# Kernel tuning notes

Measured on AMD Instinct MI355X. Metric: run time of the kernel, lower is better.

## Reference

```python
import jax, jax.numpy as jnp
import numpy as np

N = 100000      # num graph nodes
E = 1600000     # num edges (avg degree 16)
IN = 128        # in_channels
H = 128         # hidden_channels
B = 4096        # query batch
CTX = 20        # context set length (indices[:, 3:])


def setup_inputs() -> dict:
    key = jax.random.key(0)
    ks = jax.random.split(key, 16)
    inp = {
        "indices": jax.random.randint(ks[0], (B, 3 + CTX), 0, N, dtype=jnp.int64),
        "src": jax.random.randint(ks[1], (E,), 0, N, dtype=jnp.int32),
        "dst": jax.random.randint(ks[2], (E,), 0, N, dtype=jnp.int32),
        "w": jax.random.uniform(ks[3], (E,), dtype=jnp.float32),
        # learned params
        "ndata": jax.random.normal(ks[4], (N, IN), dtype=jnp.float32),
        "W1": jax.random.normal(ks[5], (H, IN), dtype=jnp.float32) * (1.0 / np.sqrt(IN)),
        "b1": jnp.zeros((H,), jnp.float32),
        "W2": jax.random.normal(ks[6], (H, H), dtype=jnp.float32) * (1.0 / np.sqrt(H)),
        "b2": jnp.zeros((H,), jnp.float32),
        "eps": jnp.zeros((2,), jnp.float32),  # learn_eps, one per GINConv
        "Wc1": jax.random.normal(ks[7], (H, 3 * H), dtype=jnp.float32) * (1.0 / np.sqrt(3 * H)),
        "bc1": jnp.zeros((H,), jnp.float32),
        "Wc2": jax.random.normal(ks[8], (H // 2, H), dtype=jnp.float32) * (1.0 / np.sqrt(H)),
        "bc2": jnp.zeros((H // 2,), jnp.float32),
        "Wc3": jax.random.normal(ks[9], (1, H // 2), dtype=jnp.float32) * (1.0 / np.sqrt(H // 2)),
        "bc3": jnp.zeros((1,), jnp.float32),
    }
    return inp


def _gin_conv(x, src, dst, w, deg, eps, W, b):
    # DGL GINConv(mean, learn_eps): h = lin((1+eps)*x + mean_{in-edges}(w_e * x_src))
    msg = w[:, None] * x[src]                                   # [E, D]
    agg = jax.ops.segment_sum(msg, dst, num_segments=N) / deg   # [N, D]
    return ((1.0 + eps) * x + agg) @ W.T + b


def reference(indices, src, dst, w, ndata, W1, b1, W2, b2, eps,
              Wc1, bc1, Wc2, bc2, Wc3, bc3):
    deg = jax.ops.segment_sum(jnp.ones((E,), ndata.dtype), dst, num_segments=N)
    deg = jnp.maximum(deg, 1.0)[:, None]

    x = ndata
    x = jax.nn.relu(_gin_conv(x, src, dst, w, deg, eps[0], W1, b1))  # dropout inactive (eval)
    x = _gin_conv(x, src, dst, w, deg, eps[1], W2, b2)               # last layer: no relu
    x = x.at[0].set(0.0)                                             # x[0] = zeros

    ing1 = x[indices[:, 0]]   # [B, H]
    ing2 = x[indices[:, 1]]   # [B, H]

    # embed_context: mean over nonzero-index context members
    ctx_idx = indices[:, 3:]                                   # [B, CTX]
    ctx_sum = x[ctx_idx].sum(axis=1)                           # [B, H]
    norm = jnp.maximum((ctx_idx > 0).sum(axis=1), 1).astype(x.dtype)[:, None]
    ctx = ctx_sum / norm

    y = jnp.concatenate([ing1, ing2, ctx], axis=1)             # [B, 3H]
    y = jax.nn.relu(y @ Wc1.T + bc1)
    y = jax.nn.relu(y @ Wc2.T + bc2)
    y = y @ Wc3.T + bc3                                        # [B, 1]
    return y
```

## Files before the change

kernel.cpp:

```cpp
#include <hip/hip_runtime.h>


#define CONV_NPB 32
#define FIN_EPB 8

__global__ void init_kernel(const float* __restrict__ W1, const float* __restrict__ W2,
                            const float* __restrict__ Wc1, const float* __restrict__ Wc2,
                            float* __restrict__ Wt1, float* __restrict__ Wt2,
                            float* __restrict__ Wc1t, float* __restrict__ Wc2t,
                            int* __restrict__ cnt, int n) {
  int i = blockIdx.x * blockDim.x + threadIdx.x;
  if (i < n) cnt[i] = 0;
  if (i < 16384) {
    int f = i >> 7, k = i & 127;
    Wt1[k * 128 + f] = W1[i];
  } else if (i < 32768) {
    int j = i - 16384; int f = j >> 7, k = j & 127;
    Wt2[k * 128 + f] = W2[j];
  } else if (i < 81920) {
    int j = i - 32768; int f = j / 384, k = j % 384;
    Wc1t[k * 128 + f] = Wc1[j];
  } else if (i < 90112) {
    int j = i - 81920; int f = j >> 7, k = j & 127;
    Wc2t[k * 64 + f] = Wc2[j];
  }
}

__global__ void hist_kernel(const int* __restrict__ dst, int* __restrict__ cnt,
                            int* __restrict__ rank, int E) {
  int e = (blockIdx.x * blockDim.x + threadIdx.x) * 4;
  if (e + 3 < E) {
    const int4 d = *(const int4*)&dst[e];
    int4 r;
    r.x = atomicAdd(&cnt[d.x], 1);
    r.y = atomicAdd(&cnt[d.y], 1);
    r.z = atomicAdd(&cnt[d.z], 1);
    r.w = atomicAdd(&cnt[d.w], 1);
    *(int4*)&rank[e] = r;
  } else {
    for (; e < E; ++e) rank[e] = atomicAdd(&cnt[dst[e]], 1);
  }
}

__global__ void scan1_kernel(const int* __restrict__ cnt, int* __restrict__ prow,
                             int* __restrict__ bsum, int n) {
  __shared__ int smem[256];
  const int t = threadIdx.x;
  const int base = blockIdx.x * 2048 + t * 8;
  int v[8];
  int s = 0;
#pragma unroll
  for (int j = 0; j < 8; ++j) {
    int idx = base + j;
    v[j] = (idx < n) ? ((cnt[idx] + 7) & ~7) : 0;
    s += v[j];
  }
  smem[t] = s;
  __syncthreads();
  for (int off = 1; off < 256; off <<= 1) {
    int add = (t >= off) ? smem[t - off] : 0;
    __syncthreads();
    smem[t] += add;
    __syncthreads();
  }
  int run = smem[t] - s;
  if (t == 255) bsum[blockIdx.x] = smem[255];
#pragma unroll
  for (int j = 0; j < 8; ++j) {
    int idx = base + j;
    if (idx < n) prow[idx] = run;
    run += v[j];
  }
}

__global__ void scan2_kernel(int* __restrict__ bsum, int nb) {
  const int t = threadIdx.x;
  if (nb <= 64) {
    const int orig = (t < nb) ? bsum[t] : 0;
    int v = orig;
#pragma unroll
    for (int off = 1; off < 64; off <<= 1) {
      int u = __shfl_up(v, off);
      if (t >= off) v += u;
    }
    if (t == nb - 1) bsum[nb] = v;
    if (t < nb) bsum[t] = v - orig;
  } else if (t == 0) {
    int run = 0;
    for (int i = 0; i < nb; ++i) { int v = bsum[i]; bsum[i] = run; run += v; }
    bsum[nb] = run;
  }
}

__global__ void scatter_kernel(const int* __restrict__ src, const int* __restrict__ dst,
                               const float* __restrict__ w, const int* __restrict__ prow,
                               const int* __restrict__ bsum, const int* __restrict__ rank,
                               const int* __restrict__ cnt,
                               int2* __restrict__ epack, int E, int n) {
  const int i = blockIdx.x * blockDim.x + threadIdx.x;
  int e = i * 4;
  if (e + 3 < E) {
    const int4 d = *(const int4*)&dst[e];
    const int4 s = *(const int4*)&src[e];
    const float4 wv = *(const float4*)&w[e];
    const int4 r = *(const int4*)&rank[e];
    epack[prow[d.x] + bsum[d.x >> 11] + r.x] = make_int2(s.x, __float_as_int(wv.x));
    epack[prow[d.y] + bsum[d.y >> 11] + r.y] = make_int2(s.y, __float_as_int(wv.y));
    epack[prow[d.z] + bsum[d.z >> 11] + r.z] = make_int2(s.z, __float_as_int(wv.z));
    epack[prow[d.w] + bsum[d.w >> 11] + r.w] = make_int2(s.w, __float_as_int(wv.w));
  } else {
    for (; e < E; ++e) {
      const int d = dst[e];
      epack[prow[d] + bsum[d >> 11] + rank[e]] = make_int2(src[e], __float_as_int(w[e]));
    }
  }
  if (i < n) {
    const int c = cnt[i];
    const int start = prow[i] + bsum[i >> 11] + c;
    const int pc = ((c + 7) & ~7) - c;
    for (int j = 0; j < pc; ++j) epack[start + j] = make_int2(0, 0);
  }
}

__launch_bounds__(256, 8)
__global__ void conv_kernel(const float* __restrict__ xin, float* __restrict__ xout,
                            const int* __restrict__ prow, const int* __restrict__ bsum,
                            const int* __restrict__ cnt,
                            const int2* __restrict__ epack,
                            const float* __restrict__ Wt,
                            const float* __restrict__ bias, const float* __restrict__ eps,
                            int epsidx, int dorelu, int zerorow0, int n, int nchunk) {
  __shared__ float xm[CONV_NPB * 128];
  __shared__ int rp_s[CONV_NPB + 1];
  const int t = threadIdx.x;
  const int nb = blockIdx.x * CONV_NPB;
  const float epsv = 1.0f + eps[epsidx];

#pragma unroll
  for (int i = 0; i < 4; ++i)
    *(float4*)&xm[(t + i * 256) * 4] = make_float4(0.f, 0.f, 0.f, 0.f);
  if (t <= CONV_NPB) {
    const int node = nb + t;
    rp_s[t] = (node >= n) ? bsum[nchunk] : (prow[node] + bsum[node >> 11]);
  }
  __syncthreads();

  {
    const int L = t >> 5;
    const int lane = t & 31;
    const int f0 = lane * 4;
    const int e0 = rp_s[0], eT = rp_s[CONV_NPB];
    const int nbat = (eT - e0) >> 3;
    const int chunk = (((nbat + 7) >> 3)) << 3;
    const int jb = e0 + L * chunk;
    const int je = min(jb + chunk, eT);
    if (jb < je) {
      const int4* ep4 = (const int4*)epack;
      int r = 0;
      while (rp_s[r + 1] <= jb) ++r;
      float4 acc = make_float4(0.f, 0.f, 0.f, 0.f);
      int h = jb >> 1;
      int4 q0 = ep4[h + 0];
      int4 q1 = ep4[h + 1];
      int4 q2 = ep4[h + 2];
      int4 q3 = ep4[h + 3];
      for (int j = jb; j < je; j += 8) {
        if (rp_s[r + 1] <= j) {
          float* bp = &xm[r * 128 + lane];
          atomicAdd(bp + 0,  acc.x);
          atomicAdd(bp + 32, acc.y);
          atomicAdd(bp + 64, acc.z);
          atomicAdd(bp + 96, acc.w);
          acc = make_float4(0.f, 0.f, 0.f, 0.f);
          do { ++r; } while (rp_s[r + 1] <= j);
        }
        const float4 a0 = *(const float4*)&xin[(size_t)q0.x * 128 + f0];
        const float4 a1 = *(const float4*)&xin[(size_t)q0.z * 128 + f0];
        const float4 a2 = *(const float4*)&xin[(size_t)q1.x * 128 + f0];
        const float4 a3 = *(const float4*)&xin[(size_t)q1.z * 128 + f0];
        const float4 a4 = *(const float4*)&xin[(size_t)q2.x * 128 + f0];
        const float4 a5 = *(const float4*)&xin[(size_t)q2.z * 128 + f0];
        const float4 a6 = *(const float4*)&xin[(size_t)q3.x * 128 + f0];
        const float4 a7 = *(const float4*)&xin[(size_t)q3.z * 128 + f0];
        const float w0 = __int_as_float(q0.y), w1 = __int_as_float(q0.w);
        const float w2 = __int_as_float(q1.y), w3 = __int_as_float(q1.w);
        const float w4 = __int_as_float(q2.y), w5 = __int_as_float(q2.w);
        const float w6 = __int_as_float(q3.y), w7 = __int_as_float(q3.w);
        const int jn = (j + 8 < je) ? (j + 8) : j;
        const int hn = jn >> 1;
        q0 = ep4[hn + 0];
        q1 = ep4[hn + 1];
        q2 = ep4[hn + 2];
        q3 = ep4[hn + 3];
        acc.x += w0 * a0.x + w1 * a1.x + w2 * a2.x + w3 * a3.x
               + w4 * a4.x + w5 * a5.x + w6 * a6.x + w7 * a7.x;
        acc.y += w0 * a0.y + w1 * a1.y + w2 * a2.y + w3 * a3.y
               + w4 * a4.y + w5 * a5.y + w6 * a6.y + w7 * a7.y;
        acc.z += w0 * a0.z + w1 * a1.z + w2 * a2.z + w3 * a3.z
               + w4 * a4.z + w5 * a5.z + w6 * a6.z + w7 * a7.z;
        acc.w += w0 * a0.w + w1 * a1.w + w2 * a2.w + w3 * a3.w
               + w4 * a4.w + w5 * a5.w + w6 * a6.w + w7 * a7.w;
      }
      float* bp = &xm[r * 128 + lane];
      atomicAdd(bp + 0,  acc.x);
      atomicAdd(bp + 32, acc.y);
      atomicAdd(bp + 64, acc.z);
      atomicAdd(bp + 96, acc.w);
    }
  }
  __syncthreads();

  {
    float4 m[4];
#pragma unroll
    for (int q = 0; q < 4; ++q) {
      const int task = t + q * 256;
      const int r = task >> 5;
      const int fg = task & 31;
      m[q].x = xm[r * 128 + fg];
      m[q].y = xm[r * 128 + 32 + fg];
      m[q].z = xm[r * 128 + 64 + fg];
      m[q].w = xm[r * 128 + 96 + fg];
    }
    __syncthreads();
#pragma unroll
    for (int q = 0; q < 4; ++q) {
      const int task = t + q * 256;
      const int r = task >> 5;
      const int fg = task & 31;
      const int f0 = fg * 4;
      const int node = nb + r;
      float4 v = make_float4(0.f, 0.f, 0.f, 0.f);
      if (node < n) {
        const int d = cnt[node];
        const float rdeg = 1.0f / (float)(d > 1 ? d : 1);
        const float4 xv = *(const float4*)&xin[(size_t)node * 128 + f0];
        v.x = epsv * xv.x + m[q].x * rdeg;
        v.y = epsv * xv.y + m[q].y * rdeg;
        v.z = epsv * xv.z + m[q].z * rdeg;
        v.w = epsv * xv.w + m[q].w * rdeg;
      }
      *(float4*)&xm[r * 128 + f0] = v;
    }
  }
  __syncthreads();

  {
    const int fg = t & 31;
    const int rg = t >> 5;
    const int f0 = fg * 4;
    const int r0 = rg * 4;
    float4 acc[4];
#pragma unroll
    for (int r = 0; r < 4; ++r) acc[r] = make_float4(0.f, 0.f, 0.f, 0.f);
    for (int k = 0; k < 128; k += 4) {
      const float4 w0 = *(const float4*)&Wt[(k + 0) * 128 + f0];
      const float4 w1 = *(const float4*)&Wt[(k + 1) * 128 + f0];
      const float4 w2 = *(const float4*)&Wt[(k + 2) * 128 + f0];
      const float4 w3 = *(const float4*)&Wt[(k + 3) * 128 + f0];
#pragma unroll
      for (int r = 0; r < 4; ++r) {
        const float4 xv = *(const float4*)&xm[(r0 + r) * 128 + k];
        acc[r].x += xv.x * w0.x + xv.y * w1.x + xv.z * w2.x + xv.w * w3.x;
        acc[r].y += xv.x * w0.y + xv.y * w1.y + xv.z * w2.y + xv.w * w3.y;
        acc[r].z += xv.x * w0.z + xv.y * w1.z + xv.z * w2.z + xv.w * w3.z;
        acc[r].w += xv.x * w0.w + xv.y * w1.w + xv.z * w2.w + xv.w * w3.w;
      }
    }
    const float4 bv = *(const float4*)&bias[f0];
#pragma unroll
    for (int r = 0; r < 4; ++r) {
      const int node = nb + r0 + r;
      if (node < n) {
        float4 v;
        v.x = acc[r].x + bv.x;
        v.y = acc[r].y + bv.y;
        v.z = acc[r].z + bv.z;
        v.w = acc[r].w + bv.w;
        if (dorelu) {
          v.x = fmaxf(v.x, 0.f); v.y = fmaxf(v.y, 0.f);
          v.z = fmaxf(v.z, 0.f); v.w = fmaxf(v.w, 0.f);
        }
        if (zerorow0 && node == 0) { v.x = 0.f; v.y = 0.f; v.z = 0.f; v.w = 0.f; }
        *(float4*)&xout[(size_t)node * 128 + f0] = v;
      }
    }
  }
}

__launch_bounds__(256, 4)
__global__ void final_kernel(const float* __restrict__ x2, const int* __restrict__ indices,
                             const float* __restrict__ Wc1t, const float* __restrict__ bc1,
                             const float* __restrict__ Wc2t, const float* __restrict__ bc2,
                             const float* __restrict__ Wc3, const float* __restrict__ bc3,
                             float* __restrict__ out) {
  __shared__ float ysm[FIN_EPB * 384];
  __shared__ float h1s[FIN_EPB * 128];
  __shared__ float h2s[FIN_EPB * 64];
  __shared__ int ind_s[FIN_EPB * 23];
  __shared__ float ccs[FIN_EPB];
  const int t = threadIdx.x;
  const int b0 = blockIdx.x * FIN_EPB;

  if (t < FIN_EPB * 23) ind_s[t] = indices[(size_t)b0 * 23 + t];
  __syncthreads();
  if (t < FIN_EPB) {
    int cc = 0;
#pragma unroll
    for (int j = 0; j < 20; ++j) cc += (ind_s[t * 23 + 3 + j] > 0) ? 1 : 0;
    ccs[t] = 1.0f / (float)(cc > 0 ? cc : 1);
  }
  __syncthreads();

  {
#pragma unroll
    for (int q = 0; q < 2; ++q) {
      const int s = t + q * 256;
      const int e = s >> 6;
      const int half = (s >> 5) & 1;
      const int fg = s & 31;
      const int idx = ind_s[e * 23 + half];
      *(float4*)&ysm[e * 384 + half * 128 + fg * 4] =
          *(const float4*)&x2[(size_t)idx * 128 + fg * 4];
    }
    const int e = t >> 5;
    const int fg = t & 31;
    float4 acc = make_float4(0.f, 0.f, 0.f, 0.f);
#pragma unroll
    for (int j = 0; j < 20; ++j) {
      const int cj = ind_s[e * 23 + 3 + j];
      const float4 a = *(const float4*)&x2[(size_t)cj * 128 + fg * 4];
      acc.x += a.x; acc.y += a.y; acc.z += a.z; acc.w += a.w;
    }
    const float sc = ccs[e];
    acc.x *= sc; acc.y *= sc; acc.z *= sc; acc.w *= sc;
    *(float4*)&ysm[e * 384 + 256 + fg * 4] = acc;
  }
  __syncthreads();

  {
    const int f1 = t & 127;
    const int eh = t >> 7;
    float acc[4];
    const float b = bc1[f1];
#pragma unroll
    for (int i = 0; i < 4; ++i) acc[i] = b;
    for (int k = 0; k < 384; k += 4) {
      const float wv0 = Wc1t[(k + 0) * 128 + f1];
      const float wv1 = Wc1t[(k + 1) * 128 + f1];
      const float wv2 = Wc1t[(k + 2) * 128 + f1];
      const float wv3 = Wc1t[(k + 3) * 128 + f1];
#pragma unroll
      for (int i = 0; i < 4; ++i) {
        const float4 yv = *(const float4*)&ysm[(eh * 4 + i) * 384 + k];
        acc[i] += yv.x * wv0 + yv.y * wv1 + yv.z * wv2 + yv.w * wv3;
      }
    }
#pragma unroll
    for (int i = 0; i < 4; ++i)
      h1s[(eh * 4 + i) * 128 + f1] = fmaxf(acc[i], 0.f);
  }
  __syncthreads();

  {
    const int f2 = t & 63;
    const int eg = t >> 6;
    float acc[2];
    const float b = bc2[f2];
#pragma unroll
    for (int i = 0; i < 2; ++i) acc[i] = b;
    for (int k = 0; k < 128; k += 4) {
      const float wv0 = Wc2t[(k + 0) * 64 + f2];
      const float wv1 = Wc2t[(k + 1) * 64 + f2];
      const float wv2 = Wc2t[(k + 2) * 64 + f2];
      const float wv3 = Wc2t[(k + 3) * 64 + f2];
#pragma unroll
      for (int i = 0; i < 2; ++i) {
        const float4 hv = *(const float4*)&h1s[(eg * 2 + i) * 128 + k];
        acc[i] += hv.x * wv0 + hv.y * wv1 + hv.z * wv2 + hv.w * wv3;
      }
    }
#pragma unroll
    for (int i = 0; i < 2; ++i)
      h2s[(eg * 2 + i) * 64 + f2] = fmaxf(acc[i], 0.f);
  }
  __syncthreads();

  {
    const int e = t >> 5;
    const int l = t & 31;
    float p = h2s[e * 64 + l] * Wc3[l] + h2s[e * 64 + l + 32] * Wc3[l + 32];
#pragma unroll
    for (int o = 16; o > 0; o >>= 1) p += __shfl_down(p, o, 32);
    if (l == 0) out[b0 + e] = p + bc3[0];
  }
}

extern "C" void kernel_launch(void* const* d_in, const int* in_sizes, int n_in,
                              void* d_out, int out_size, void* d_ws, size_t ws_size,
                              hipStream_t stream) {
  const int* indices = (const int*)d_in[0];
  const int* src = (const int*)d_in[1];
  const int* dst = (const int*)d_in[2];
  const float* w = (const float*)d_in[3];
  const float* ndata = (const float*)d_in[4];
  const float* W1 = (const float*)d_in[5];
  const float* b1 = (const float*)d_in[6];
  const float* W2 = (const float*)d_in[7];
  const float* b2 = (const float*)d_in[8];
  const float* eps = (const float*)d_in[9];
  const float* Wc1 = (const float*)d_in[10];
  const float* bc1 = (const float*)d_in[11];
  const float* Wc2 = (const float*)d_in[12];
  const float* bc2 = (const float*)d_in[13];
  const float* Wc3 = (const float*)d_in[14];
  const float* bc3 = (const float*)d_in[15];
  float* out = (float*)d_out;

  const int E = in_sizes[1];
  const int N = in_sizes[4] / 128;
  const int B = in_sizes[0] / 23;

  char* ws = (char*)d_ws;
  size_t off = 0;
  auto alloc = [&](size_t bytes) -> char* {
    char* p = ws + off;
    off = (off + bytes + 255) & ~(size_t)255;
    return p;
  };
  const size_t Epad = (size_t)E + 8 * (size_t)N;
  int* cnt = (int*)alloc((size_t)N * 4);
  int* prow = (int*)alloc((size_t)(N + 1) * 4);
  int* rank = (int*)alloc((size_t)E * 4);
  int* bsum = (int*)alloc(256 * 4);
  int2* epack = (int2*)alloc(Epad * 8);
  float* x1 = (float*)alloc((size_t)N * 128 * 4);
  float* x2 = (float*)alloc((size_t)N * 128 * 4);
  float* Wt1 = (float*)alloc(16384 * 4);
  float* Wt2 = (float*)alloc(16384 * 4);
  float* Wc1t = (float*)alloc(49152 * 4);
  float* Wc2t = (float*)alloc(8192 * 4);

  const int ninit = (N > 90112) ? N : 90112;
  init_kernel<<<(ninit + 255) / 256, 256, 0, stream>>>(W1, W2, Wc1, Wc2, Wt1, Wt2, Wc1t, Wc2t, cnt, N);
  const int Eq = (E + 3) / 4;
  hist_kernel<<<(Eq + 255) / 256, 256, 0, stream>>>(dst, cnt, rank, E);
  const int nchunk = (N + 2047) / 2048;
  scan1_kernel<<<nchunk, 256, 0, stream>>>(cnt, prow, bsum, N);
  scan2_kernel<<<1, 64, 0, stream>>>(bsum, nchunk);
  const int nsc = (Eq > N) ? Eq : N;
  scatter_kernel<<<(nsc + 255) / 256, 256, 0, stream>>>(src, dst, w, prow, bsum, rank, cnt, epack, E, N);

  const int nconv = (N + CONV_NPB - 1) / CONV_NPB;
  conv_kernel<<<nconv, 256, 0, stream>>>(ndata, x1, prow, bsum, cnt, epack, Wt1, b1, eps, 0, 1, 0, N, nchunk);
  conv_kernel<<<nconv, 256, 0, stream>>>(x1, x2, prow, bsum, cnt, epack, Wt2, b2, eps, 1, 0, 1, N, nchunk);

  final_kernel<<<B / FIN_EPB, 256, 0, stream>>>(x2, indices, Wc1t, bc1, Wc2t, bc2, Wc3, bc3, out);
}
```

Measured before the change: 554.1 us.

## Gather neighbor features in fp16 to halve edge-gather bandwidth

Node features are kept as fp16 copies: ndata is cast during init, and each conv layer writes an fp16 output alongside (or instead of) fp32. The edge gather in the aggregation and the final context gather read the half-precision rows and convert them to float for accumulation. This halves the random-access gather traffic, which is the dominant cost. In exchange it adds a cast pass over ndata, an extra fp16 store in layer 1, and rounding error in the aggregated features.

```diff
diff --git a/kernel.cpp b/kernel.cpp
--- a/kernel.cpp
+++ b/kernel.cpp
@@ -1,16 +1,41 @@
 #include <hip/hip_runtime.h>
+#include <hip/hip_fp16.h>
 
 
 #define CONV_NPB 32
 #define FIN_EPB 8
 
+struct __align__(8)  h4 { __half2 a, b; };
+struct __align__(16) h8 { __half2 a, b, c, d; };
+
+__device__ __forceinline__ float4 h4f(h4 u) {
+  return make_float4(__low2float(u.a), __high2float(u.a),
+                     __low2float(u.b), __high2float(u.b));
+}
+__device__ __forceinline__ h4 f4h(float4 v) {
+  h4 u; u.a = __floats2half2_rn(v.x, v.y); u.b = __floats2half2_rn(v.z, v.w);
+  return u;
+}
+
 __global__ void init_kernel(const float* __restrict__ W1, const float* __restrict__ W2,
                             const float* __restrict__ Wc1, const float* __restrict__ Wc2,
+                            const float* __restrict__ ndata, __half* __restrict__ xh0,
                             float* __restrict__ Wt1, float* __restrict__ Wt2,
                             float* __restrict__ Wc1t, float* __restrict__ Wc2t,
                             int* __restrict__ cnt, int n) {
   int i = blockIdx.x * blockDim.x + threadIdx.x;
   if (i < n) cnt[i] = 0;
+  const int cbase = i * 8;
+  if (cbase < n * 128) {
+    const float4 v0 = *(const float4*)&ndata[cbase];
+    const float4 v1 = *(const float4*)&ndata[cbase + 4];
+    h8 u;
+    u.a = __floats2half2_rn(v0.x, v0.y);
+    u.b = __floats2half2_rn(v0.z, v0.w);
+    u.c = __floats2half2_rn(v1.x, v1.y);
+    u.d = __floats2half2_rn(v1.z, v1.w);
+    *(h8*)&xh0[cbase] = u;
+  }
   if (i < 16384) {
     int f = i >> 7, k = i & 127;
     Wt1[k * 128 + f] = W1[i];
@@ -123,13 +148,15 @@
 }
 
 __launch_bounds__(256, 8)
-__global__ void conv_kernel(const float* __restrict__ xin, float* __restrict__ xout,
+__global__ void conv_kernel(const float* __restrict__ xin, const __half* __restrict__ xinh,
+                            float* __restrict__ xout, __half* __restrict__ xouth,
                             const int* __restrict__ prow, const int* __restrict__ bsum,
                             const int* __restrict__ cnt,
                             const int2* __restrict__ epack,
                             const float* __restrict__ Wt,
                             const float* __restrict__ bias, const float* __restrict__ eps,
-                            int epsidx, int dorelu, int zerorow0, int n, int nchunk) {
+                            int epsidx, int dorelu, int zerorow0, int writef32,
+                            int n, int nchunk) {
   __shared__ float xm[CONV_NPB * 128];
   __shared__ int rp_s[CONV_NPB + 1];
   const int t = threadIdx.x;
@@ -174,14 +201,14 @@
           acc = make_float4(0.f, 0.f, 0.f, 0.f);
           do { ++r; } while (rp_s[r + 1] <= j);
         }
-        const float4 a0 = *(const float4*)&xin[(size_t)q0.x * 128 + f0];
-        const float4 a1 = *(const float4*)&xin[(size_t)q0.z * 128 + f0];
-        const float4 a2 = *(const float4*)&xin[(size_t)q1.x * 128 + f0];
-        const float4 a3 = *(const float4*)&xin[(size_t)q1.z * 128 + f0];
-        const float4 a4 = *(const float4*)&xin[(size_t)q2.x * 128 + f0];
-        const float4 a5 = *(const float4*)&xin[(size_t)q2.z * 128 + f0];
-        const float4 a6 = *(const float4*)&xin[(size_t)q3.x * 128 + f0];
-        const float4 a7 = *(const float4*)&xin[(size_t)q3.z * 128 + f0];
+        const h4 u0 = *(const h4*)&xinh[(size_t)q0.x * 128 + f0];
+        const h4 u1 = *(const h4*)&xinh[(size_t)q0.z * 128 + f0];
+        const h4 u2 = *(const h4*)&xinh[(size_t)q1.x * 128 + f0];
+        const h4 u3 = *(const h4*)&xinh[(size_t)q1.z * 128 + f0];
+        const h4 u4 = *(const h4*)&xinh[(size_t)q2.x * 128 + f0];
+        const h4 u5 = *(const h4*)&xinh[(size_t)q2.z * 128 + f0];
+        const h4 u6 = *(const h4*)&xinh[(size_t)q3.x * 128 + f0];
+        const h4 u7 = *(const h4*)&xinh[(size_t)q3.z * 128 + f0];
         const float w0 = __int_as_float(q0.y), w1 = __int_as_float(q0.w);
         const float w2 = __int_as_float(q1.y), w3 = __int_as_float(q1.w);
         const float w4 = __int_as_float(q2.y), w5 = __int_as_float(q2.w);
@@ -192,6 +219,8 @@
         q1 = ep4[hn + 1];
         q2 = ep4[hn + 2];
         q3 = ep4[hn + 3];
+        const float4 a0 = h4f(u0), a1 = h4f(u1), a2 = h4f(u2), a3 = h4f(u3);
+        const float4 a4 = h4f(u4), a5 = h4f(u5), a6 = h4f(u6), a7 = h4f(u7);
         acc.x += w0 * a0.x + w1 * a1.x + w2 * a2.x + w3 * a3.x
                + w4 * a4.x + w5 * a5.x + w6 * a6.x + w7 * a7.x;
         acc.y += w0 * a0.y + w1 * a1.y + w2 * a2.y + w3 * a3.y
@@ -282,14 +311,15 @@
           v.z = fmaxf(v.z, 0.f); v.w = fmaxf(v.w, 0.f);
         }
         if (zerorow0 && node == 0) { v.x = 0.f; v.y = 0.f; v.z = 0.f; v.w = 0.f; }
-        *(float4*)&xout[(size_t)node * 128 + f0] = v;
+        *(h4*)&xouth[(size_t)node * 128 + f0] = f4h(v);
+        if (writef32) *(float4*)&xout[(size_t)node * 128 + f0] = v;
       }
     }
   }
 }
 
 __launch_bounds__(256, 4)
-__global__ void final_kernel(const float* __restrict__ x2, const int* __restrict__ indices,
+__global__ void final_kernel(const __half* __restrict__ x2h, const int* __restrict__ indices,
                              const float* __restrict__ Wc1t, const float* __restrict__ bc1,
                              const float* __restrict__ Wc2t, const float* __restrict__ bc2,
                              const float* __restrict__ Wc3, const float* __restrict__ bc3,
@@ -317,11 +347,11 @@
     for (int q = 0; q < 2; ++q) {
       const int s = t + q * 256;
       const int e = s >> 6;
-      const int half = (s >> 5) & 1;
+      const int hf = (s >> 5) & 1;
       const int fg = s & 31;
-      const int idx = ind_s[e * 23 + half];
-      *(float4*)&ysm[e * 384 + half * 128 + fg * 4] =
-          *(const float4*)&x2[(size_t)idx * 128 + fg * 4];
+      const int idx = ind_s[e * 23 + hf];
+      const h4 u = *(const h4*)&x2h[(size_t)idx * 128 + fg * 4];
+      *(float4*)&ysm[e * 384 + hf * 128 + fg * 4] = h4f(u);
     }
     const int e = t >> 5;
     const int fg = t & 31;
@@ -329,7 +359,8 @@
 #pragma unroll
     for (int j = 0; j < 20; ++j) {
       const int cj = ind_s[e * 23 + 3 + j];
-      const float4 a = *(const float4*)&x2[(size_t)cj * 128 + fg * 4];
+      const h4 u = *(const h4*)&x2h[(size_t)cj * 128 + fg * 4];
+      const float4 a = h4f(u);
       acc.x += a.x; acc.y += a.y; acc.z += a.z; acc.w += a.w;
     }
     const float sc = ccs[e];
@@ -435,14 +466,19 @@
   int* bsum = (int*)alloc(256 * 4);
   int2* epack = (int2*)alloc(Epad * 8);
   float* x1 = (float*)alloc((size_t)N * 128 * 4);
-  float* x2 = (float*)alloc((size_t)N * 128 * 4);
+  __half* xh0 = (__half*)alloc((size_t)N * 128 * 2);
+  __half* x1h = (__half*)alloc((size_t)N * 128 * 2);
   float* Wt1 = (float*)alloc(16384 * 4);
   float* Wt2 = (float*)alloc(16384 * 4);
   float* Wc1t = (float*)alloc(49152 * 4);
   float* Wc2t = (float*)alloc(8192 * 4);
-
-  const int ninit = (N > 90112) ? N : 90112;
-  init_kernel<<<(ninit + 255) / 256, 256, 0, stream>>>(W1, W2, Wc1, Wc2, Wt1, Wt2, Wc1t, Wc2t, cnt, N);
+  __half* x2h = xh0;
+
+  const int ncast = (N * 128 + 7) / 8;
+  int ninit = (N > 90112) ? N : 90112;
+  if (ncast > ninit) ninit = ncast;
+  init_kernel<<<(ninit + 255) / 256, 256, 0, stream>>>(W1, W2, Wc1, Wc2, ndata, xh0,
+                                                       Wt1, Wt2, Wc1t, Wc2t, cnt, N);
   const int Eq = (E + 3) / 4;
   hist_kernel<<<(Eq + 255) / 256, 256, 0, stream>>>(dst, cnt, rank, E);
   const int nchunk = (N + 2047) / 2048;
@@ -452,8 +488,10 @@
   scatter_kernel<<<(nsc + 255) / 256, 256, 0, stream>>>(src, dst, w, prow, bsum, rank, cnt, epack, E, N);
 
   const int nconv = (N + CONV_NPB - 1) / CONV_NPB;
-  conv_kernel<<<nconv, 256, 0, stream>>>(ndata, x1, prow, bsum, cnt, epack, Wt1, b1, eps, 0, 1, 0, N, nchunk);
-  conv_kernel<<<nconv, 256, 0, stream>>>(x1, x2, prow, bsum, cnt, epack, Wt2, b2, eps, 1, 0, 1, N, nchunk);
-
-  final_kernel<<<B / FIN_EPB, 256, 0, stream>>>(x2, indices, Wc1t, bc1, Wc2t, bc2, Wc3, bc3, out);
-}
+  conv_kernel<<<nconv, 256, 0, stream>>>(ndata, xh0, x1, x1h, prow, bsum, cnt, epack,
+                                         Wt1, b1, eps, 0, 1, 0, 1, N, nchunk);
+  conv_kernel<<<nconv, 256, 0, stream>>>(x1, x1h, nullptr, x2h, prow, bsum, cnt, epack,
+                                         Wt2, b2, eps, 1, 0, 1, 0, N, nchunk);
+
+  final_kernel<<<B / FIN_EPB, 256, 0, stream>>>(x2h, indices, Wc1t, bc1, Wc2t, bc2, Wc3, bc3, out);
+}
```

Result: faster. 513.7 us (-7.3%).
